# Optimization experiments

Measured on AMD Instinct MI355X. Metric: run time of the kernel, lower is better.

The kernel has to match this reference:

```python
import jax, jax.numpy as jnp
import numpy as np
from jax.ops import segment_sum

N, E, F, H, G, T = 50000, 800000, 128, 256, 512, 4


def setup_inputs() -> dict:
    key = jax.random.key(0)
    ks = jax.random.split(key, 12)
    x = jax.random.normal(ks[0], (N, F), jnp.float32)
    edge_index = jax.random.randint(ks[1], (2, E), 0, N)
    batch = jnp.sort(jax.random.randint(ks[2], (N,), 0, G))
    num_atoms = jax.random.normal(ks[3], (G, 1), jnp.float32)
    def lin(k, fan_in, fan_out):
        s = 1.0 / np.sqrt(fan_in)
        return jax.random.uniform(k, (fan_in, fan_out), jnp.float32, -s, s)
    W1 = lin(ks[4], F, H); b1 = jnp.zeros((H,), jnp.float32)
    W2 = lin(ks[5], H, H); b2 = jnp.zeros((H,), jnp.float32)
    W3 = lin(ks[6], H + 1, 32); b3 = jnp.zeros((32,), jnp.float32)
    W4 = lin(ks[7], 32, T); b4 = jnp.zeros((T,), jnp.float32)
    return {"x": x, "edge_index": edge_index, "batch": batch, "num_atoms": num_atoms,
            "W1": W1, "b1": b1, "W2": W2, "b2": b2, "W3": W3, "b3": b3, "W4": W4, "b4": b4}


def _gcn_norm(edge_index, num_nodes):
    # PyG GCNConv default: add self-loops, symmetric D^-1/2 A D^-1/2 normalization
    loop = jnp.arange(num_nodes, dtype=edge_index.dtype)
    src = jnp.concatenate([edge_index[0], loop])
    dst = jnp.concatenate([edge_index[1], loop])
    deg = segment_sum(jnp.ones_like(dst, jnp.float32), dst, num_segments=num_nodes)
    dinv = jnp.where(deg > 0, jax.lax.rsqrt(jnp.maximum(deg, 1e-12)), 0.0)
    norm = dinv[src] * dinv[dst]  # [E+N]
    return src, dst, norm


def _gcn_conv(x, W, b, src, dst, norm, num_nodes):
    h = x @ W  # [N, out]
    agg = segment_sum(h[src] * norm[:, None], dst, num_segments=num_nodes)
    return agg + b


def reference(x, edge_index, batch, num_atoms, W1, b1, W2, b2, W3, b3, W4, b4):
    n = x.shape[0]
    src, dst, norm = _gcn_norm(edge_index, n)
    h = jax.nn.relu(_gcn_conv(x, W1, b1, src, dst, norm, n))   # dropout = identity (eval)
    h = jax.nn.relu(_gcn_conv(h, W2, b2, src, dst, norm, n))
    # global mean pool over graphs
    sums = segment_sum(h, batch, num_segments=G)               # [G, H]
    cnt = segment_sum(jnp.ones((n,), jnp.float32), batch, num_segments=G)
    pooled = sums / jnp.maximum(cnt, 1.0)[:, None]
    z = jnp.concatenate([pooled, num_atoms], axis=1)           # [G, H+1]
    z = jax.nn.relu(z @ W3 + b3)
    return z @ W4 + b4                                         # [G, T]
```

## Files before the change

kernel.cpp:

```cpp
#include <hip/hip_runtime.h>
#include <hip/hip_bf16.h>


#define NN 50000
#define EE 800000
#define FDIM 128
#define HDIM 256
#define GG 512
#define SCAN_NB ((NN + 255) / 256)

typedef __attribute__((ext_vector_type(8))) short short8;
typedef __attribute__((ext_vector_type(4))) float floatx4;

__device__ __forceinline__ unsigned short f2bf(float f) {
    unsigned u = __float_as_uint(f);
    return (unsigned short)((u + 0x7FFF + ((u >> 16) & 1)) >> 16);
}
__device__ __forceinline__ float bflo(unsigned v) { return __uint_as_float(v << 16); }
__device__ __forceinline__ float bfhi(unsigned v) { return __uint_as_float(v & 0xFFFF0000u); }


__global__ void hist_kernel(const int* __restrict__ dst, int* __restrict__ deg, int e) {
    int i = blockIdx.x * blockDim.x + threadIdx.x;
    int stride = gridDim.x * blockDim.x;
    for (; i < e; i += stride) atomicAdd(&deg[dst[i]], 1);
}

__global__ __launch_bounds__(256) void scan_part(const int* __restrict__ deg,
                                                 int* __restrict__ row_off,
                                                 int* __restrict__ blk_sums,
                                                 float* __restrict__ dinv, int n) {
    __shared__ int s[256];
    int tid = threadIdx.x;
    int i = blockIdx.x * 256 + tid;
    int v = (i < n) ? deg[i] : 0;
    if (i < n) dinv[i] = rsqrtf((float)v + 1.0f);
    s[tid] = v;
    __syncthreads();
    #pragma unroll
    for (int off = 1; off < 256; off <<= 1) {
        int t = (tid >= off) ? s[tid - off] : 0;
        __syncthreads();
        s[tid] += t;
        __syncthreads();
    }
    if (i < n) row_off[i] = s[tid] - v;
    if (tid == 255) blk_sums[blockIdx.x] = s[255];
}

__global__ __launch_bounds__(256) void scan_sums(int* __restrict__ blk_sums, int nb) {
    __shared__ int s[256];
    int tid = threadIdx.x;
    int v = (tid < nb) ? blk_sums[tid] : 0;
    s[tid] = v;
    __syncthreads();
    #pragma unroll
    for (int off = 1; off < 256; off <<= 1) {
        int t = (tid >= off) ? s[tid - off] : 0;
        __syncthreads();
        s[tid] += t;
        __syncthreads();
    }
    if (tid < nb) blk_sums[tid] = s[tid] - v;
}

__global__ __launch_bounds__(256) void scan_add(int* __restrict__ row_off,
                                                const int* __restrict__ blk_sums,
                                                int* __restrict__ fill, int n, int e) {
    int i = blockIdx.x * 256 + threadIdx.x;
    if (i < n) {
        row_off[i] += blk_sums[blockIdx.x];
        fill[i] = 0;
    }
    if (i == 0) row_off[n] = e;
}

__global__ void scatter_kernel(const int* __restrict__ src, const int* __restrict__ dst,
                               const int* __restrict__ row_off, int* __restrict__ fill,
                               const float* __restrict__ dinv,
                               int2* __restrict__ csr, int e) {
    int i = blockIdx.x * blockDim.x + threadIdx.x;
    int stride = gridDim.x * blockDim.x;
    for (; i < e; i += stride) {
        int s = src[i], d = dst[i];
        int pos = row_off[d] + atomicAdd(&fill[d], 1);
        csr[pos] = make_int2(s, __float_as_int(dinv[s] * dinv[d]));
    }
}

__global__ void cast_f32_bf16(const float* __restrict__ in, unsigned short* __restrict__ out,
                              int count) {
    int i = (blockIdx.x * blockDim.x + threadIdx.x) * 4;
    int stride = gridDim.x * blockDim.x * 4;
    for (; i < count; i += stride) {
        float4 v = *(const float4*)&in[i];
        ushort4 o;
        o.x = f2bf(v.x); o.y = f2bf(v.y); o.z = f2bf(v.z); o.w = f2bf(v.w);
        *(ushort4*)&out[i] = o;
    }
}

__global__ void transpose_cast_bf16(const float* __restrict__ W, unsigned short* __restrict__ Wt,
                                    int K, int Nc) {
    int idx = blockIdx.x * blockDim.x + threadIdx.x;
    if (idx < K * Nc) {
        int nn = idx / K, k = idx - nn * K;
        Wt[idx] = f2bf(W[(size_t)k * Nc + nn]);
    }
}


#define FMA8(v, wgt) do { unsigned _u; \
    _u = (unsigned)(v).x; acc0 = fmaf(bflo(_u), (wgt), acc0); acc1 = fmaf(bfhi(_u), (wgt), acc1); \
    _u = (unsigned)(v).y; acc2 = fmaf(bflo(_u), (wgt), acc2); acc3 = fmaf(bfhi(_u), (wgt), acc3); \
    _u = (unsigned)(v).z; acc4 = fmaf(bflo(_u), (wgt), acc4); acc5 = fmaf(bfhi(_u), (wgt), acc5); \
    _u = (unsigned)(v).w; acc6 = fmaf(bflo(_u), (wgt), acc6); acc7 = fmaf(bfhi(_u), (wgt), acc7); } while (0)

__global__ __launch_bounds__(256) void gcn_agg256_bf16(const unsigned short* __restrict__ in,
                                                       const int* __restrict__ row_off,
                                                       const int2* __restrict__ csr,
                                                       const float* __restrict__ dinv,
                                                       unsigned short* __restrict__ out, int n) {
    int wave = threadIdx.x >> 6;
    int lane = threadIdx.x & 63;
    int node = blockIdx.x * 4 + wave;
    if (node >= n) return;
    int sub = lane >> 5;
    int fl  = lane & 31;
    float di = dinv[node];
    float w0 = (sub == 0) ? di * di : 0.f;

    float acc0, acc1, acc2, acc3, acc4, acc5, acc6, acc7;
    {
        int4 sv = *(const int4*)&in[(size_t)node * 256 + fl * 8];
        unsigned _u;
        _u = (unsigned)sv.x; acc0 = bflo(_u) * w0; acc1 = bfhi(_u) * w0;
        _u = (unsigned)sv.y; acc2 = bflo(_u) * w0; acc3 = bfhi(_u) * w0;
        _u = (unsigned)sv.z; acc4 = bflo(_u) * w0; acc5 = bfhi(_u) * w0;
        _u = (unsigned)sv.w; acc6 = bflo(_u) * w0; acc7 = bfhi(_u) * w0;
    }

    int beg = __builtin_amdgcn_readfirstlane(row_off[node]);
    int end = __builtin_amdgcn_readfirstlane(row_off[node + 1]);
    int cnt = end - beg;
    if (cnt > 0) {
        int nIter = (cnt + 7) >> 3;
        int base = beg;
        int last = end - 1;
        int i0 = base + 0 + sub, i1 = base + 2 + sub, i2 = base + 4 + sub, i3 = base + 6 + sub;
        int2 c0 = csr[i0 < end ? i0 : last];
        int2 c1 = csr[i1 < end ? i1 : last];
        int2 c2 = csr[i2 < end ? i2 : last];
        int2 c3 = csr[i3 < end ? i3 : last];
        for (int it = 0; it < nIter; ++it) {
            int4 g0 = *(const int4*)&in[(size_t)c0.x * 256 + fl * 8];
            int4 g1 = *(const int4*)&in[(size_t)c1.x * 256 + fl * 8];
            int4 g2 = *(const int4*)&in[(size_t)c2.x * 256 + fl * 8];
            int4 g3 = *(const int4*)&in[(size_t)c3.x * 256 + fl * 8];
            float we0 = (base + 0 + sub < end) ? __int_as_float(c0.y) : 0.f;
            float we1 = (base + 2 + sub < end) ? __int_as_float(c1.y) : 0.f;
            float we2 = (base + 4 + sub < end) ? __int_as_float(c2.y) : 0.f;
            float we3 = (base + 6 + sub < end) ? __int_as_float(c3.y) : 0.f;
            int nb = base + 8;
            int j0 = nb + 0 + sub, j1 = nb + 2 + sub, j2 = nb + 4 + sub, j3 = nb + 6 + sub;
            int2 n0 = csr[j0 < end ? j0 : last];
            int2 n1 = csr[j1 < end ? j1 : last];
            int2 n2 = csr[j2 < end ? j2 : last];
            int2 n3 = csr[j3 < end ? j3 : last];
            FMA8(g0, we0); FMA8(g1, we1); FMA8(g2, we2); FMA8(g3, we3);
            c0 = n0; c1 = n1; c2 = n2; c3 = n3; base = nb;
        }
    }
    acc0 += __shfl_xor(acc0, 32); acc1 += __shfl_xor(acc1, 32);
    acc2 += __shfl_xor(acc2, 32); acc3 += __shfl_xor(acc3, 32);
    acc4 += __shfl_xor(acc4, 32); acc5 += __shfl_xor(acc5, 32);
    acc6 += __shfl_xor(acc6, 32); acc7 += __shfl_xor(acc7, 32);
    if (sub == 0) {
        int4 o;
        o.x = (int)((unsigned)f2bf(acc0) | ((unsigned)f2bf(acc1) << 16));
        o.y = (int)((unsigned)f2bf(acc2) | ((unsigned)f2bf(acc3) << 16));
        o.z = (int)((unsigned)f2bf(acc4) | ((unsigned)f2bf(acc5) << 16));
        o.w = (int)((unsigned)f2bf(acc6) | ((unsigned)f2bf(acc7) << 16));
        *(int4*)&out[(size_t)node * 256 + fl * 8] = o;
    }
}

__global__ __launch_bounds__(256) void gcn_agg128_bf16(const unsigned short* __restrict__ in,
                                                       const int* __restrict__ row_off,
                                                       const int2* __restrict__ csr,
                                                       const float* __restrict__ dinv,
                                                       unsigned short* __restrict__ out, int n) {
    int wave = threadIdx.x >> 6;
    int lane = threadIdx.x & 63;
    int node = blockIdx.x * 4 + wave;
    if (node >= n) return;
    int sub = lane >> 4;
    int fl  = lane & 15;
    float di = dinv[node];
    float w0 = (sub == 0) ? di * di : 0.f;

    float acc0, acc1, acc2, acc3, acc4, acc5, acc6, acc7;
    {
        int4 sv = *(const int4*)&in[(size_t)node * 128 + fl * 8];
        unsigned _u;
        _u = (unsigned)sv.x; acc0 = bflo(_u) * w0; acc1 = bfhi(_u) * w0;
        _u = (unsigned)sv.y; acc2 = bflo(_u) * w0; acc3 = bfhi(_u) * w0;
        _u = (unsigned)sv.z; acc4 = bflo(_u) * w0; acc5 = bfhi(_u) * w0;
        _u = (unsigned)sv.w; acc6 = bflo(_u) * w0; acc7 = bfhi(_u) * w0;
    }

    int beg = __builtin_amdgcn_readfirstlane(row_off[node]);
    int end = __builtin_amdgcn_readfirstlane(row_off[node + 1]);
    int cnt = end - beg;
    if (cnt > 0) {
        int nIter = (cnt + 7) >> 3;
        int base = beg;
        int last = end - 1;
        int i0 = base + sub, i1 = base + 4 + sub;
        int2 c0 = csr[i0 < end ? i0 : last];
        int2 c1 = csr[i1 < end ? i1 : last];
        for (int it = 0; it < nIter; ++it) {
            int4 g0 = *(const int4*)&in[(size_t)c0.x * 128 + fl * 8];
            int4 g1 = *(const int4*)&in[(size_t)c1.x * 128 + fl * 8];
            float we0 = (base + sub < end) ? __int_as_float(c0.y) : 0.f;
            float we1 = (base + 4 + sub < end) ? __int_as_float(c1.y) : 0.f;
            int nb = base + 8;
            int j0 = nb + sub, j1 = nb + 4 + sub;
            int2 n0 = csr[j0 < end ? j0 : last];
            int2 n1 = csr[j1 < end ? j1 : last];
            FMA8(g0, we0); FMA8(g1, we1);
            c0 = n0; c1 = n1; base = nb;
        }
    }
    acc0 += __shfl_xor(acc0, 16); acc1 += __shfl_xor(acc1, 16);
    acc2 += __shfl_xor(acc2, 16); acc3 += __shfl_xor(acc3, 16);
    acc4 += __shfl_xor(acc4, 16); acc5 += __shfl_xor(acc5, 16);
    acc6 += __shfl_xor(acc6, 16); acc7 += __shfl_xor(acc7, 16);
    acc0 += __shfl_xor(acc0, 32); acc1 += __shfl_xor(acc1, 32);
    acc2 += __shfl_xor(acc2, 32); acc3 += __shfl_xor(acc3, 32);
    acc4 += __shfl_xor(acc4, 32); acc5 += __shfl_xor(acc5, 32);
    acc6 += __shfl_xor(acc6, 32); acc7 += __shfl_xor(acc7, 32);
    if (sub == 0) {
        int4 o;
        o.x = (int)((unsigned)f2bf(acc0) | ((unsigned)f2bf(acc1) << 16));
        o.y = (int)((unsigned)f2bf(acc2) | ((unsigned)f2bf(acc3) << 16));
        o.z = (int)((unsigned)f2bf(acc4) | ((unsigned)f2bf(acc5) << 16));
        o.w = (int)((unsigned)f2bf(acc6) | ((unsigned)f2bf(acc7) << 16));
        *(int4*)&out[(size_t)node * 128 + fl * 8] = o;
    }
}


__global__ __launch_bounds__(512, 4) void gemm1_mfma_bias_relu(
        const unsigned short* __restrict__ A,
        const unsigned short* __restrict__ Bt,
        const float* __restrict__ bias,
        unsigned short* __restrict__ C, int M) {
    constexpr int K = FDIM, Nc = HDIM, LDT = 40;
    __shared__ unsigned short As[128 * LDT];
    __shared__ unsigned short Bs[256 * LDT];
    int tid = threadIdx.x;
    int lane = tid & 63, wave = tid >> 6;
    int wm = (wave >> 2) * 64, wn = (wave & 3) * 64;
    int bm = blockIdx.x * 128;
    int l15 = lane & 15, quad = lane >> 4;

    floatx4 zero = {0.f, 0.f, 0.f, 0.f};
    floatx4 acc[4][4];
    #pragma unroll
    for (int s = 0; s < 4; ++s)
        #pragma unroll
        for (int t = 0; t < 4; ++t) acc[s][t] = zero;

    for (int k0 = 0; k0 < K; k0 += 32) {
        {
            int row = tid >> 2, q = tid & 3;
            int4 va = {0, 0, 0, 0};
            int gr = bm + row;
            if (gr < M) va = *(const int4*)&A[(size_t)gr * K + k0 + q * 8];
            *(int4*)&As[row * LDT + q * 8] = va;
        }
        #pragma unroll
        for (int c = tid; c < 1024; c += 512) {
            int row = c >> 2, q = c & 3;
            int4 vb = *(const int4*)&Bt[(size_t)row * K + k0 + q * 8];
            *(int4*)&Bs[row * LDT + q * 8] = vb;
        }
        __syncthreads();
        short8 af[4], bf[4];
        #pragma unroll
        for (int s = 0; s < 4; ++s)
            af[s] = *(const short8*)&As[(wm + s * 16 + l15) * LDT + quad * 8];
        #pragma unroll
        for (int t = 0; t < 4; ++t)
            bf[t] = *(const short8*)&Bs[(wn + t * 16 + l15) * LDT + quad * 8];
        #pragma unroll
        for (int s = 0; s < 4; ++s)
            #pragma unroll
            for (int t = 0; t < 4; ++t)
                acc[s][t] = __builtin_amdgcn_mfma_f32_16x16x32_bf16(af[s], bf[t], acc[s][t], 0, 0, 0);
        __syncthreads();
    }
    #pragma unroll
    for (int s = 0; s < 4; ++s) {
        int row0 = bm + wm + s * 16 + quad * 4;
        #pragma unroll
        for (int t = 0; t < 4; ++t) {
            int col = wn + t * 16 + l15;
            float bb = bias[col];
            #pragma unroll
            for (int r = 0; r < 4; ++r) {
                int row = row0 + r;
                if (row < M)
                    C[(size_t)row * Nc + col] = f2bf(fmaxf(acc[s][t][r] + bb, 0.f));
            }
        }
    }
}

__global__ __launch_bounds__(512, 4) void gemm2_pool(
        const unsigned short* __restrict__ A,
        const unsigned short* __restrict__ Bt,
        const float* __restrict__ bias,
        const int* __restrict__ batch,
        float* __restrict__ pool, int M) {
    constexpr int K = HDIM, Nc = HDIM, LDT = 40;
    __shared__ unsigned short As[128 * LDT];
    __shared__ unsigned short Bs[256 * LDT];
    int tid = threadIdx.x;
    int lane = tid & 63, wave = tid >> 6;
    int wm = (wave >> 2) * 64, wn = (wave & 3) * 64;
    int bm = blockIdx.x * 128;
    int l15 = lane & 15, quad = lane >> 4;

    floatx4 zero = {0.f, 0.f, 0.f, 0.f};
    floatx4 acc[4][4];
    #pragma unroll
    for (int s = 0; s < 4; ++s)
        #pragma unroll
        for (int t = 0; t < 4; ++t) acc[s][t] = zero;

    for (int k0 = 0; k0 < K; k0 += 32) {
        {
            int row = tid >> 2, q = tid & 3;
            int4 va = {0, 0, 0, 0};
            int gr = bm + row;
            if (gr < M) va = *(const int4*)&A[(size_t)gr * K + k0 + q * 8];
            *(int4*)&As[row * LDT + q * 8] = va;
        }
        #pragma unroll
        for (int c = tid; c < 1024; c += 512) {
            int row = c >> 2, q = c & 3;
            int4 vb = *(const int4*)&Bt[(size_t)row * K + k0 + q * 8];
            *(int4*)&Bs[row * LDT + q * 8] = vb;
        }
        __syncthreads();
        short8 af[4], bf[4];
        #pragma unroll
        for (int s = 0; s < 4; ++s)
            af[s] = *(const short8*)&As[(wm + s * 16 + l15) * LDT + quad * 8];
        #pragma unroll
        for (int t = 0; t < 4; ++t)
            bf[t] = *(const short8*)&Bs[(wn + t * 16 + l15) * LDT + quad * 8];
        #pragma unroll
        for (int s = 0; s < 4; ++s)
            #pragma unroll
            for (int t = 0; t < 4; ++t)
                acc[s][t] = __builtin_amdgcn_mfma_f32_16x16x32_bf16(af[s], bf[t], acc[s][t], 0, 0, 0);
        __syncthreads();
    }
    #pragma unroll
    for (int s = 0; s < 4; ++s) {
        int row0 = bm + wm + s * 16 + quad * 4;
        if (row0 >= M) continue;
        bool full = (row0 + 3 < M);
        int gA = batch[row0];
        int gB = full ? batch[row0 + 3] : gA;
        bool same = full && (gA == gB);
        #pragma unroll
        for (int t = 0; t < 4; ++t) {
            int col = wn + t * 16 + l15;
            float bb = bias[col];
            if (same) {
                float v = fmaxf(acc[s][t][0] + bb, 0.f) + fmaxf(acc[s][t][1] + bb, 0.f)
                        + fmaxf(acc[s][t][2] + bb, 0.f) + fmaxf(acc[s][t][3] + bb, 0.f);
                atomicAdd(&pool[(size_t)gA * Nc + col], v);
            } else {
                #pragma unroll
                for (int r = 0; r < 4; ++r) {
                    int row = row0 + r;
                    if (row < M) {
                        float v = fmaxf(acc[s][t][r] + bb, 0.f);
                        atomicAdd(&pool[(size_t)batch[row] * Nc + col], v);
                    }
                }
            }
        }
    }
}


__device__ __forceinline__ int lower_bound_i(const int* __restrict__ a, int n, int v) {
    int lo = 0, hi = n;
    while (lo < hi) {
        int mid = (lo + hi) >> 1;
        if (a[mid] < v) lo = mid + 1; else hi = mid;
    }
    return lo;
}

__global__ __launch_bounds__(256) void head_kernel(const float* __restrict__ pool,
                                                   const int* __restrict__ batch,
                                                   const float* __restrict__ num_atoms,
                                                   const float* __restrict__ W3, const float* __restrict__ b3,
                                                   const float* __restrict__ W4, const float* __restrict__ b4,
                                                   float* __restrict__ out, int n) {
    int g = blockIdx.x;
    int tid = threadIdx.x;
    __shared__ int s_lo, s_hi;
    if (tid == 0) {
        s_lo = lower_bound_i(batch, n, g);
        s_hi = lower_bound_i(batch, n, g + 1);
    }
    __syncthreads();
    float cnt = (float)(s_hi - s_lo);

    __shared__ float zin[HDIM + 1];
    __shared__ float z[32];
    zin[tid] = pool[(size_t)g * HDIM + tid] / fmaxf(cnt, 1.0f);
    if (tid == 0) zin[HDIM] = num_atoms[g];
    __syncthreads();
    if (tid < 32) {
        float a = b3[tid];
        for (int k = 0; k < HDIM + 1; ++k) a = fmaf(zin[k], W3[k * 32 + tid], a);
        z[tid] = fmaxf(a, 0.f);
    }
    __syncthreads();
    if (tid < 4) {
        float a = b4[tid];
        #pragma unroll
        for (int k = 0; k < 32; ++k) a = fmaf(z[k], W4[k * 4 + tid], a);
        out[g * 4 + tid] = a;
    }
}


extern "C" void kernel_launch(void* const* d_in, const int* in_sizes, int n_in,
                              void* d_out, int out_size, void* d_ws, size_t ws_size,
                              hipStream_t stream) {
    const float* x         = (const float*)d_in[0];
    const int*   edge_idx  = (const int*)d_in[1];
    const int*   batch     = (const int*)d_in[2];
    const float* num_atoms = (const float*)d_in[3];
    const float* W1 = (const float*)d_in[4];
    const float* b1 = (const float*)d_in[5];
    const float* W2 = (const float*)d_in[6];
    const float* b2 = (const float*)d_in[7];
    const float* W3 = (const float*)d_in[8];
    const float* b3 = (const float*)d_in[9];
    const float* W4 = (const float*)d_in[10];
    const float* b4 = (const float*)d_in[11];
    float* out = (float*)d_out;

    const int n = NN, e = EE;
    const int* e_src = edge_idx;
    const int* e_dst = edge_idx + e;

    char* ws = (char*)d_ws;
    size_t off = 0;
    auto carve = [&](size_t bytes) -> void* {
        void* p = ws + off;
        off = (off + bytes + 255) & ~(size_t)255;
        return p;
    };
    int*   deg_i    = (int*)carve((size_t)n * 4);
    int*   row_off  = (int*)carve((size_t)(n + 1) * 4);
    int*   fill     = (int*)carve((size_t)n * 4);
    int*   blk_sums = (int*)carve((size_t)256 * 4);
    float* dinv     = (float*)carve((size_t)n * 4);
    unsigned short* W1t = (unsigned short*)carve((size_t)FDIM * HDIM * 2);
    unsigned short* W2t = (unsigned short*)carve((size_t)HDIM * HDIM * 2);
    int2*  csr      = (int2*)carve((size_t)e * 8);
    unsigned short* P = (unsigned short*)carve((size_t)n * HDIM * 2);
    unsigned short* Q = (unsigned short*)carve((size_t)n * HDIM * 2);
    float* pool     = (float*)carve((size_t)GG * HDIM * 4);
    unsigned short* x_bf = P;
    unsigned short* a0b  = P + (size_t)n * FDIM;
    unsigned short* a1b  = P;
    unsigned short* h1b  = Q;
    (void)ws_size; (void)n_in; (void)in_sizes; (void)out_size;

    hipMemsetAsync(deg_i, 0, (size_t)n * 4, stream);
    hipMemsetAsync(pool, 0, (size_t)GG * HDIM * 4, stream);
    hist_kernel<<<1024, 256, 0, stream>>>(e_dst, deg_i, e);
    scan_part<<<SCAN_NB, 256, 0, stream>>>(deg_i, row_off, blk_sums, dinv, n);
    scan_sums<<<1, 256, 0, stream>>>(blk_sums, SCAN_NB);
    scan_add<<<SCAN_NB, 256, 0, stream>>>(row_off, blk_sums, fill, n, e);
    scatter_kernel<<<1024, 256, 0, stream>>>(e_src, e_dst, row_off, fill, dinv, csr, e);

    cast_f32_bf16<<<1024, 256, 0, stream>>>(x, x_bf, n * FDIM);
    transpose_cast_bf16<<<(FDIM * HDIM + 255) / 256, 256, 0, stream>>>(W1, W1t, FDIM, HDIM);
    transpose_cast_bf16<<<(HDIM * HDIM + 255) / 256, 256, 0, stream>>>(W2, W2t, HDIM, HDIM);

    int gemm_grid = (n + 127) / 128;
    gcn_agg128_bf16<<<(n + 3) / 4, 256, 0, stream>>>(x_bf, row_off, csr, dinv, a0b, n);
    gemm1_mfma_bias_relu<<<gemm_grid, 512, 0, stream>>>(a0b, W1t, b1, h1b, n);
    gcn_agg256_bf16<<<(n + 3) / 4, 256, 0, stream>>>(h1b, row_off, csr, dinv, a1b, n);
    gemm2_pool<<<gemm_grid, 512, 0, stream>>>(a1b, W2t, b2, batch, pool, n);
    head_kernel<<<GG, 256, 0, stream>>>(pool, batch, num_atoms, W3, b3, W4, b4, out, n);
}
```

Baseline: 354.9 us.

## Split aggregation across feature slices with 16 edges per wave iteration

```diff
diff --git a/kernel.cpp b/kernel.cpp
--- a/kernel.cpp
+++ b/kernel.cpp
@@ -116,137 +116,54 @@
     _u = (unsigned)(v).z; acc4 = fmaf(bflo(_u), (wgt), acc4); acc5 = fmaf(bfhi(_u), (wgt), acc5); \
     _u = (unsigned)(v).w; acc6 = fmaf(bflo(_u), (wgt), acc6); acc7 = fmaf(bfhi(_u), (wgt), acc7); } while (0)
 
-__global__ __launch_bounds__(256) void gcn_agg256_bf16(const unsigned short* __restrict__ in,
-                                                       const int* __restrict__ row_off,
-                                                       const int2* __restrict__ csr,
-                                                       const float* __restrict__ dinv,
-                                                       unsigned short* __restrict__ out, int n) {
+template<int ROWU, int LOGS>
+__global__ __launch_bounds__(256) void gcn_agg_sliced(const unsigned short* __restrict__ in,
+                                                      const int* __restrict__ row_off,
+                                                      const int2* __restrict__ csr,
+                                                      const float* __restrict__ dinv,
+                                                      unsigned short* __restrict__ out, int n) {
     int wave = threadIdx.x >> 6;
     int lane = threadIdx.x & 63;
-    int node = blockIdx.x * 4 + wave;
+    int slice = blockIdx.x & ((1 << LOGS) - 1);
+    int node = (blockIdx.x >> LOGS) * 4 + wave;
     if (node >= n) return;
-    int sub = lane >> 5;
-    int fl  = lane & 31;
-    float di = dinv[node];
-    float w0 = (sub == 0) ? di * di : 0.f;
-
-    float acc0, acc1, acc2, acc3, acc4, acc5, acc6, acc7;
-    {
-        int4 sv = *(const int4*)&in[(size_t)node * 256 + fl * 8];
-        unsigned _u;
-        _u = (unsigned)sv.x; acc0 = bflo(_u) * w0; acc1 = bfhi(_u) * w0;
-        _u = (unsigned)sv.y; acc2 = bflo(_u) * w0; acc3 = bfhi(_u) * w0;
-        _u = (unsigned)sv.z; acc4 = bflo(_u) * w0; acc5 = bfhi(_u) * w0;
-        _u = (unsigned)sv.w; acc6 = bflo(_u) * w0; acc7 = bfhi(_u) * w0;
-    }
+    int es = lane >> 2;
+    int fc = lane & 3;
+    int colu = slice * 32 + fc * 8;
+
+    float acc0 = 0.f, acc1 = 0.f, acc2 = 0.f, acc3 = 0.f;
+    float acc4 = 0.f, acc5 = 0.f, acc6 = 0.f, acc7 = 0.f;
 
     int beg = __builtin_amdgcn_readfirstlane(row_off[node]);
     int end = __builtin_amdgcn_readfirstlane(row_off[node + 1]);
-    int cnt = end - beg;
-    if (cnt > 0) {
-        int nIter = (cnt + 7) >> 3;
-        int base = beg;
+    if (end > beg) {
         int last = end - 1;
-        int i0 = base + 0 + sub, i1 = base + 2 + sub, i2 = base + 4 + sub, i3 = base + 6 + sub;
-        int2 c0 = csr[i0 < end ? i0 : last];
-        int2 c1 = csr[i1 < end ? i1 : last];
-        int2 c2 = csr[i2 < end ? i2 : last];
-        int2 c3 = csr[i3 < end ? i3 : last];
-        for (int it = 0; it < nIter; ++it) {
-            int4 g0 = *(const int4*)&in[(size_t)c0.x * 256 + fl * 8];
-            int4 g1 = *(const int4*)&in[(size_t)c1.x * 256 + fl * 8];
-            int4 g2 = *(const int4*)&in[(size_t)c2.x * 256 + fl * 8];
-            int4 g3 = *(const int4*)&in[(size_t)c3.x * 256 + fl * 8];
-            float we0 = (base + 0 + sub < end) ? __int_as_float(c0.y) : 0.f;
-            float we1 = (base + 2 + sub < end) ? __int_as_float(c1.y) : 0.f;
-            float we2 = (base + 4 + sub < end) ? __int_as_float(c2.y) : 0.f;
-            float we3 = (base + 6 + sub < end) ? __int_as_float(c3.y) : 0.f;
-            int nb = base + 8;
-            int j0 = nb + 0 + sub, j1 = nb + 2 + sub, j2 = nb + 4 + sub, j3 = nb + 6 + sub;
-            int2 n0 = csr[j0 < end ? j0 : last];
-            int2 n1 = csr[j1 < end ? j1 : last];
-            int2 n2 = csr[j2 < end ? j2 : last];
-            int2 n3 = csr[j3 < end ? j3 : last];
-            FMA8(g0, we0); FMA8(g1, we1); FMA8(g2, we2); FMA8(g3, we3);
-            c0 = n0; c1 = n1; c2 = n2; c3 = n3; base = nb;
-        }
-    }
-    acc0 += __shfl_xor(acc0, 32); acc1 += __shfl_xor(acc1, 32);
-    acc2 += __shfl_xor(acc2, 32); acc3 += __shfl_xor(acc3, 32);
-    acc4 += __shfl_xor(acc4, 32); acc5 += __shfl_xor(acc5, 32);
-    acc6 += __shfl_xor(acc6, 32); acc7 += __shfl_xor(acc7, 32);
-    if (sub == 0) {
+        for (int base = beg; base < end; base += 16) {
+            int idx = base + es;
+            int2 c = csr[idx < end ? idx : last];
+            float wgt = (idx < end) ? __int_as_float(c.y) : 0.f;
+            int4 g = *(const int4*)&in[(size_t)c.x * ROWU + colu];
+            FMA8(g, wgt);
+        }
+    }
+    #pragma unroll
+    for (int m = 4; m <= 32; m <<= 1) {
+        acc0 += __shfl_xor(acc0, m); acc1 += __shfl_xor(acc1, m);
+        acc2 += __shfl_xor(acc2, m); acc3 += __shfl_xor(acc3, m);
+        acc4 += __shfl_xor(acc4, m); acc5 += __shfl_xor(acc5, m);
+        acc6 += __shfl_xor(acc6, m); acc7 += __shfl_xor(acc7, m);
+    }
+    if (es == 0) {
+        float di = dinv[node];
+        float w0 = di * di;
+        int4 sv = *(const int4*)&in[(size_t)node * ROWU + colu];
+        FMA8(sv, w0);
         int4 o;
         o.x = (int)((unsigned)f2bf(acc0) | ((unsigned)f2bf(acc1) << 16));
         o.y = (int)((unsigned)f2bf(acc2) | ((unsigned)f2bf(acc3) << 16));
         o.z = (int)((unsigned)f2bf(acc4) | ((unsigned)f2bf(acc5) << 16));
         o.w = (int)((unsigned)f2bf(acc6) | ((unsigned)f2bf(acc7) << 16));
-        *(int4*)&out[(size_t)node * 256 + fl * 8] = o;
-    }
-}
-
-__global__ __launch_bounds__(256) void gcn_agg128_bf16(const unsigned short* __restrict__ in,
-                                                       const int* __restrict__ row_off,
-                                                       const int2* __restrict__ csr,
-                                                       const float* __restrict__ dinv,
-                                                       unsigned short* __restrict__ out, int n) {
-    int wave = threadIdx.x >> 6;
-    int lane = threadIdx.x & 63;
-    int node = blockIdx.x * 4 + wave;
-    if (node >= n) return;
-    int sub = lane >> 4;
-    int fl  = lane & 15;
-    float di = dinv[node];
-    float w0 = (sub == 0) ? di * di : 0.f;
-
-    float acc0, acc1, acc2, acc3, acc4, acc5, acc6, acc7;
-    {
-        int4 sv = *(const int4*)&in[(size_t)node * 128 + fl * 8];
-        unsigned _u;
-        _u = (unsigned)sv.x; acc0 = bflo(_u) * w0; acc1 = bfhi(_u) * w0;
-        _u = (unsigned)sv.y; acc2 = bflo(_u) * w0; acc3 = bfhi(_u) * w0;
-        _u = (unsigned)sv.z; acc4 = bflo(_u) * w0; acc5 = bfhi(_u) * w0;
-        _u = (unsigned)sv.w; acc6 = bflo(_u) * w0; acc7 = bfhi(_u) * w0;
-    }
-
-    int beg = __builtin_amdgcn_readfirstlane(row_off[node]);
-    int end = __builtin_amdgcn_readfirstlane(row_off[node + 1]);
-    int cnt = end - beg;
-    if (cnt > 0) {
-        int nIter = (cnt + 7) >> 3;
-        int base = beg;
-        int last = end - 1;
-        int i0 = base + sub, i1 = base + 4 + sub;
-        int2 c0 = csr[i0 < end ? i0 : last];
-        int2 c1 = csr[i1 < end ? i1 : last];
-        for (int it = 0; it < nIter; ++it) {
-            int4 g0 = *(const int4*)&in[(size_t)c0.x * 128 + fl * 8];
-            int4 g1 = *(const int4*)&in[(size_t)c1.x * 128 + fl * 8];
-            float we0 = (base + sub < end) ? __int_as_float(c0.y) : 0.f;
-            float we1 = (base + 4 + sub < end) ? __int_as_float(c1.y) : 0.f;
-            int nb = base + 8;
-            int j0 = nb + sub, j1 = nb + 4 + sub;
-            int2 n0 = csr[j0 < end ? j0 : last];
-            int2 n1 = csr[j1 < end ? j1 : last];
-            FMA8(g0, we0); FMA8(g1, we1);
-            c0 = n0; c1 = n1; base = nb;
-        }
-    }
-    acc0 += __shfl_xor(acc0, 16); acc1 += __shfl_xor(acc1, 16);
-    acc2 += __shfl_xor(acc2, 16); acc3 += __shfl_xor(acc3, 16);
-    acc4 += __shfl_xor(acc4, 16); acc5 += __shfl_xor(acc5, 16);
-    acc6 += __shfl_xor(acc6, 16); acc7 += __shfl_xor(acc7, 16);
-    acc0 += __shfl_xor(acc0, 32); acc1 += __shfl_xor(acc1, 32);
-    acc2 += __shfl_xor(acc2, 32); acc3 += __shfl_xor(acc3, 32);
-    acc4 += __shfl_xor(acc4, 32); acc5 += __shfl_xor(acc5, 32);
-    acc6 += __shfl_xor(acc6, 32); acc7 += __shfl_xor(acc7, 32);
-    if (sub == 0) {
-        int4 o;
-        o.x = (int)((unsigned)f2bf(acc0) | ((unsigned)f2bf(acc1) << 16));
-        o.y = (int)((unsigned)f2bf(acc2) | ((unsigned)f2bf(acc3) << 16));
-        o.z = (int)((unsigned)f2bf(acc4) | ((unsigned)f2bf(acc5) << 16));
-        o.w = (int)((unsigned)f2bf(acc6) | ((unsigned)f2bf(acc7) << 16));
-        *(int4*)&out[(size_t)node * 128 + fl * 8] = o;
+        *(int4*)&out[(size_t)node * ROWU + colu] = o;
     }
 }
 
@@ -503,9 +420,10 @@
     transpose_cast_bf16<<<(HDIM * HDIM + 255) / 256, 256, 0, stream>>>(W2, W2t, HDIM, HDIM);
 
     int gemm_grid = (n + 127) / 128;
-    gcn_agg128_bf16<<<(n + 3) / 4, 256, 0, stream>>>(x_bf, row_off, csr, dinv, a0b, n);
+    int ngroups = (n + 3) / 4;
+    gcn_agg_sliced<FDIM, 2><<<ngroups * 4, 256, 0, stream>>>(x_bf, row_off, csr, dinv, a0b, n);
     gemm1_mfma_bias_relu<<<gemm_grid, 512, 0, stream>>>(a0b, W1t, b1, h1b, n);
-    gcn_agg256_bf16<<<(n + 3) / 4, 256, 0, stream>>>(h1b, row_off, csr, dinv, a1b, n);
+    gcn_agg_sliced<HDIM, 3><<<ngroups * 8, 256, 0, stream>>>(h1b, row_off, csr, dinv, a1b, n);
     gemm2_pool<<<gemm_grid, 512, 0, stream>>>(a1b, W2t, b2, batch, pool, n);
     head_kernel<<<GG, 256, 0, stream>>>(pool, batch, num_atoms, W3, b3, W4, b4, out, n);
 }
```

Result: slower. 489.1 us (+37.8%).
